# Kernel optimization log

Hardware: AMD Instinct MI355X
Metric: run time of the kernel (lower is better)

Reference implementation:

```python
import jax, jax.numpy as jnp
import numpy as np

B, N, C = 16, 256, 2048
CLASSES = (16, 5, 5)
H = len(CLASSES)
EPS = 1e-5


def setup_inputs() -> dict:
    key = jax.random.key(0)
    ks = iter(jax.random.split(key, 32))
    d = {}
    d["features"] = jax.random.normal(next(ks), (B, N, C), dtype=jnp.float32)
    # 3 hidden conv layers per head; 3x3 conv on 1x1 spatial == linear with center tap.
    # Stack the H heads' weights: [H, C_out, C_in].
    std = 1.0 / np.sqrt(C)
    for i in (1, 2, 3):
        d[f"W{i}"] = jax.random.normal(next(ks), (H, C, C), dtype=jnp.float32) * std
        d[f"g{i}"] = 1.0 + 0.1 * jax.random.normal(next(ks), (H, C), dtype=jnp.float32)
        d[f"b{i}"] = 0.1 * jax.random.normal(next(ks), (H, C), dtype=jnp.float32)
        d[f"m{i}"] = 0.1 * jax.random.normal(next(ks), (H, C), dtype=jnp.float32)
        d[f"v{i}"] = jax.random.uniform(next(ks), (H, C), dtype=jnp.float32, minval=0.5, maxval=1.5)
    # Final 1x1 conv per head: [c_i, C] weight + [c_i] bias (output dims differ per head).
    for h, c in enumerate(CLASSES):
        d[f"Wf{h}"] = jax.random.normal(next(ks), (c, C), dtype=jnp.float32) * std
        d[f"bf{h}"] = 0.1 * jax.random.normal(next(ks), (c,), dtype=jnp.float32)
    return d


def _bn_relu(y, g, b, m, v):
    # y: [H, M, C]; per-head inference-mode BN folded to scale/shift, then ReLU.
    scale = g / jnp.sqrt(v + EPS)          # [H, C]
    shift = b - m * scale                  # [H, C]
    return jax.nn.relu(y * scale[:, None, :] + shift[:, None, :])


def reference(features, W1, g1, b1, m1, v1, W2, g2, b2, m2, v2, W3, g3, b3, m3, v3,
              Wf0, bf0, Wf1, bf1, Wf2, bf2):
    Bs, Ns, Cs = features.shape
    x = features.reshape(Bs * Ns, Cs)                       # [M, C]
    y = jnp.einsum("mc,hdc->hmd", x, W1)                    # [H, M, C]
    y = _bn_relu(y, g1, b1, m1, v1)
    y = jnp.einsum("hmc,hdc->hmd", y, W2)
    y = _bn_relu(y, g2, b2, m2, v2)
    y = jnp.einsum("hmc,hdc->hmd", y, W3)
    y = _bn_relu(y, g3, b3, m3, v3)
    outs = [y[h] @ Wf.T + bf for h, (Wf, bf) in enumerate([(Wf0, bf0), (Wf1, bf1), (Wf2, bf2)])]
    cl = jnp.concatenate(outs, axis=-1)                     # [M, sum(classes)]
    return cl.reshape(Bs, Ns, cl.shape[-1])
```

## Files before the change

### kernel.cpp

```cpp
#include <hip/hip_runtime.h>
#include <hip/hip_bf16.h>

typedef __attribute__((ext_vector_type(8))) short short8;
typedef __attribute__((ext_vector_type(4))) float f32x4;

#define BN_EPS 1e-5f
#define MROWS 4096
#define CDIM 2048
#define NKT 32

#define SB() __builtin_amdgcn_sched_barrier(0)

__device__ __forceinline__ void gload_lds16(const void* g, void* l) {
  __builtin_amdgcn_global_load_lds(
      (const __attribute__((address_space(1))) void*)g,
      (__attribute__((address_space(3))) void*)l, 16, 0, 0);
}

__global__ __launch_bounds__(256) void cvt_f32_bf16(const float* __restrict__ in,
                                                    unsigned short* __restrict__ out,
                                                    int n4) {
  int idx = blockIdx.x * blockDim.x + threadIdx.x;
  int stride = gridDim.x * blockDim.x;
  for (int i = idx; i < n4; i += stride) {
    float4 vv = ((const float4*)in)[i];
    __hip_bfloat16 h0 = __float2bfloat16(vv.x);
    __hip_bfloat16 h1 = __float2bfloat16(vv.y);
    __hip_bfloat16 h2 = __float2bfloat16(vv.z);
    __hip_bfloat16 h3 = __float2bfloat16(vv.w);
    ushort4 o;
    o.x = *(unsigned short*)&h0;
    o.y = *(unsigned short*)&h1;
    o.z = *(unsigned short*)&h2;
    o.w = *(unsigned short*)&h3;
    ((ushort4*)out)[i] = o;
  }
}

__global__ __launch_bounds__(512, 2) void gemm256_bn_relu(
    const __hip_bfloat16* __restrict__ A, long long a_hstride,
    const __hip_bfloat16* __restrict__ W,
    const float* __restrict__ gp, const float* __restrict__ bp,
    const float* __restrict__ mp, const float* __restrict__ vp,
    __hip_bfloat16* __restrict__ out)
{
  __shared__ __hip_bfloat16 sm[65536];

  const int tid  = threadIdx.x;
  const int w    = tid >> 6;
  const int lane = tid & 63;

  const int bid = blockIdx.x;
  const int swz = (bid & 7) * 48 + (bid >> 3);
  const int h   = swz >> 7;
  const int mt  = (swz & 127) >> 3;
  const int nt  = swz & 7;

  const __hip_bfloat16* Abase = A + (size_t)h * (size_t)a_hstride + (size_t)(mt * 256) * CDIM;
  const __hip_bfloat16* Bbase = W + ((size_t)h * CDIM + (size_t)(nt * 256)) * CDIM;

  const int slot0 = w * 128 + lane;
  const int srow  = slot0 >> 3;
  const int gcol  = ((slot0 & 7) ^ (srow & 7)) << 3;

  const int wm = w >> 2;
  const int wn = w & 3;
  const int fr = lane & 15;
  const int fg = lane >> 4;
  const int offs0 = fr * 64 + ((fg ^ (fr & 7)) << 3);
  const int offs1 = fr * 64 + (((fg + 4) ^ (fr & 7)) << 3);
  const int aOff = wm * 8192;
  const int bOff = 16384 + (wn >> 1) * 8192 + (wn & 1) * 4096;

  auto STAGE = [&](int dbuf, int mat, int ih, int t) {
    const __hip_bfloat16* sp = (mat ? Bbase : Abase)
        + (size_t)(ih * 128 + srow) * CDIM + t * 64 + gcol;
    __hip_bfloat16* dp = &sm[dbuf * 32768 + mat * 16384 + ih * 8192 + w * 1024];
    gload_lds16(sp, dp);
    gload_lds16(sp + 8 * CDIM, dp + 512);
  };

  f32x4 acc[8][4] = {};
  short8 A0[4], A1[4], B0[2], B1[2];

  const __hip_bfloat16* aB[2] = { &sm[aOff], &sm[32768 + aOff] };
  const __hip_bfloat16* bB[2] = { &sm[bOff], &sm[32768 + bOff] };

#define LDA(dst, base, i0, offs)                                        \
  _Pragma("unroll") for (int i_ = 0; i_ < 4; ++i_)                      \
    dst[i_] = *(const short8*)((base) + ((i0) + i_) * 1024 + (offs));
#define LDB(dst, base, j0, offs)                                        \
  _Pragma("unroll") for (int j_ = 0; j_ < 2; ++j_)                      \
    dst[j_] = *(const short8*)((base) + ((j0) + j_) * 1024 + (offs));

#define MFMA_Q(ioff, joff, Aset, Bset)                                  \
  __builtin_amdgcn_s_setprio(1);                                        \
  _Pragma("unroll") for (int i_ = 0; i_ < 4; ++i_)                      \
  _Pragma("unroll") for (int j_ = 0; j_ < 2; ++j_)                      \
    acc[i_ + ioff][j_ + joff] = __builtin_amdgcn_mfma_f32_16x16x32_bf16( \
        Aset[i_], Bset[j_], acc[i_ + ioff][j_ + joff], 0, 0, 0);        \
  __builtin_amdgcn_s_setprio(0);

  STAGE(0, 0, 0, 0); STAGE(0, 0, 1, 0); STAGE(0, 1, 0, 0); STAGE(0, 1, 1, 0);
  STAGE(1, 0, 0, 1);
  asm volatile("s_waitcnt vmcnt(2)" ::: "memory");
  SB();
  __builtin_amdgcn_s_barrier();
  SB();
  LDA(A0, aB[0], 0, offs0);
  LDA(A1, aB[0], 4, offs0);
  LDB(B0, bB[0], 0, offs0);
  LDB(B1, bB[0], 2, offs0);
  SB();

#pragma unroll 2
  for (int t = 0; t < NKT - 1; ++t) {
    const int d = t & 1, dn = d ^ 1;
    const __hip_bfloat16* aHd = aB[d];
    const __hip_bfloat16* bHd = bB[d];
    const __hip_bfloat16* aHn = aB[dn];
    const __hip_bfloat16* bHn = bB[dn];

    MFMA_Q(0, 0, A0, B0); SB();
    STAGE(dn, 0, 1, t + 1); SB();
    MFMA_Q(0, 2, A0, B1); SB();
    LDA(A0, aHd, 0, offs1); SB();
    MFMA_Q(4, 0, A1, B0); SB();
    STAGE(dn, 1, 0, t + 1);
    LDB(B0, bHd, 0, offs1); SB();
    MFMA_Q(4, 2, A1, B1); SB();
    STAGE(dn, 1, 1, t + 1);
    LDB(B1, bHd, 2, offs1);
    LDA(A1, aHd, 4, offs1); SB();
    MFMA_Q(0, 0, A0, B0); SB();
    if (t + 2 < NKT) { STAGE(d, 0, 0, t + 2); }
    SB();
    MFMA_Q(0, 2, A0, B1); SB();
    if (t + 2 < NKT) { asm volatile("s_waitcnt vmcnt(6)" ::: "memory"); }
    else             { asm volatile("s_waitcnt vmcnt(4)" ::: "memory"); }
    SB();
    __builtin_amdgcn_s_barrier();
    SB();
    LDA(A0, aHn, 0, offs0); SB();
    MFMA_Q(4, 0, A1, B0); SB();
    if (t + 2 < NKT) { asm volatile("s_waitcnt vmcnt(2)" ::: "memory"); }
    else             { asm volatile("s_waitcnt vmcnt(0)" ::: "memory"); }
    SB();
    __builtin_amdgcn_s_barrier();
    SB();
    LDB(B0, bHn, 0, offs0); SB();
    MFMA_Q(4, 2, A1, B1); SB();
    LDB(B1, bHn, 2, offs0);
    LDA(A1, aHn, 4, offs0); SB();
  }

  {
    const int d = (NKT - 1) & 1;
    const __hip_bfloat16* aHd = aB[d];
    const __hip_bfloat16* bHd = bB[d];
    MFMA_Q(0, 0, A0, B0); SB();
    MFMA_Q(0, 2, A0, B1); SB();
    LDA(A0, aHd, 0, offs1); SB();
    MFMA_Q(4, 0, A1, B0); SB();
    LDB(B0, bHd, 0, offs1); SB();
    MFMA_Q(4, 2, A1, B1); SB();
    LDB(B1, bHd, 2, offs1);
    LDA(A1, aHd, 4, offs1); SB();
    MFMA_Q(0, 0, A0, B0); SB();
    MFMA_Q(0, 2, A0, B1); SB();
    MFMA_Q(4, 0, A1, B0); SB();
    MFMA_Q(4, 2, A1, B1); SB();
  }

  const float* gh = gp + h * CDIM;
  const float* bh = bp + h * CDIM;
  const float* mh = mp + h * CDIM;
  const float* vh = vp + h * CDIM;
  const int colBase = nt * 256 + wn * 64 + fr;
  const int rowBase = mt * 256 + wm * 128 + fg * 4;
#pragma unroll
  for (int j = 0; j < 4; ++j) {
    const int col = colBase + j * 16;
    const float sc = gh[col] / sqrtf(vh[col] + BN_EPS);
    const float sh = bh[col] - mh[col] * sc;
#pragma unroll
    for (int i = 0; i < 8; ++i) {
      const int row = rowBase + i * 16;
#pragma unroll
      for (int rr = 0; rr < 4; ++rr) {
        float val = acc[i][j][rr] * sc + sh;
        val = val > 0.f ? val : 0.f;
        out[((size_t)h * MROWS + row + rr) * CDIM + col] = __float2bfloat16(val);
      }
    }
  }
}

__global__ __launch_bounds__(256) void pack_wf(
    const float* __restrict__ Wf0, const float* __restrict__ Wf1,
    const float* __restrict__ Wf2, __hip_bfloat16* __restrict__ Wfb) {
  int idx = blockIdx.x * 256 + threadIdx.x;
  if (idx >= 3 * 16 * CDIM) return;
  int h = idx / (16 * CDIM);
  int rem = idx - h * 16 * CDIM;
  int j = rem / CDIM;
  int k = rem - j * CDIM;
  float v = 0.f;
  if (h == 0)            v = Wf0[j * CDIM + k];
  else if (h == 1)       { if (j < 5) v = Wf1[j * CDIM + k]; }
  else                   { if (j < 5) v = Wf2[j * CDIM + k]; }
  Wfb[idx] = __float2bfloat16(v);
}

__global__ __launch_bounds__(512) void final_mfma(
    const __hip_bfloat16* __restrict__ act,
    const __hip_bfloat16* __restrict__ Wfb,
    const float* __restrict__ bf0, const float* __restrict__ bf1,
    const float* __restrict__ bf2, float* __restrict__ out)
{
  __shared__ float red[8][3][256];
  const int tid  = threadIdx.x;
  const int w    = tid >> 6;
  const int lane = tid & 63;
  const int r0   = blockIdx.x * 16;
  const int fr   = lane & 15;
  const int fk   = (lane >> 4) * 8;
  const int kbase = w * 256 + fk;

  f32x4 acc[3] = {};
  const __hip_bfloat16* aRow = act + (size_t)(r0 + fr) * CDIM + kbase;
  const __hip_bfloat16* bRow = Wfb + (size_t)fr * CDIM + kbase;
#pragma unroll
  for (int ks = 0; ks < 8; ++ks) {
    const int k = ks * 32;
#pragma unroll
    for (int h = 0; h < 3; ++h) {
      short8 a = *(const short8*)(aRow + (size_t)h * MROWS * CDIM + k);
      short8 b = *(const short8*)(bRow + h * 16 * CDIM + k);
      acc[h] = __builtin_amdgcn_mfma_f32_16x16x32_bf16(a, b, acc[h], 0, 0, 0);
    }
  }

  const int rb = (lane >> 4) * 4;
#pragma unroll
  for (int h = 0; h < 3; ++h)
#pragma unroll
    for (int r = 0; r < 4; ++r)
      red[w][h][(rb + r) * 16 + fr] = acc[h][r];
  __syncthreads();

  for (int e = tid; e < 768; e += 512) {
    const int h = e >> 8, idx = e & 255;
    const int row = idx >> 4, col = idx & 15;
    float s = 0.f;
#pragma unroll
    for (int w2 = 0; w2 < 8; ++w2) s += red[w2][h][idx];
    float* orow = out + (size_t)(r0 + row) * 26;
    if (h == 0)                 orow[col]      = s + bf0[col];
    else if (h == 1) { if (col < 5) orow[16 + col] = s + bf1[col]; }
    else             { if (col < 5) orow[21 + col] = s + bf2[col]; }
  }
}

extern "C" void kernel_launch(void* const* d_in, const int* in_sizes, int n_in,
                              void* d_out, int out_size, void* d_ws, size_t ws_size,
                              hipStream_t stream) {
  const float* feat = (const float*)d_in[0];
  const float* W1 = (const float*)d_in[1];
  const float* g1 = (const float*)d_in[2];
  const float* b1 = (const float*)d_in[3];
  const float* m1 = (const float*)d_in[4];
  const float* v1 = (const float*)d_in[5];
  const float* W2 = (const float*)d_in[6];
  const float* g2 = (const float*)d_in[7];
  const float* b2 = (const float*)d_in[8];
  const float* m2 = (const float*)d_in[9];
  const float* v2 = (const float*)d_in[10];
  const float* W3 = (const float*)d_in[11];
  const float* g3 = (const float*)d_in[12];
  const float* b3 = (const float*)d_in[13];
  const float* m3 = (const float*)d_in[14];
  const float* v3 = (const float*)d_in[15];
  const float* Wf0 = (const float*)d_in[16];
  const float* bf0 = (const float*)d_in[17];
  const float* Wf1 = (const float*)d_in[18];
  const float* bf1 = (const float*)d_in[19];
  const float* Wf2 = (const float*)d_in[20];
  const float* bf2 = (const float*)d_in[21];
  float* out = (float*)d_out;

  char* ws = (char*)d_ws;
  __hip_bfloat16* wbuf = (__hip_bfloat16*)ws;
  __hip_bfloat16* actA = (__hip_bfloat16*)(ws + 25165824);
  __hip_bfloat16* actB = (__hip_bfloat16*)(ws + 25165824 + 50331648);
  __hip_bfloat16* xb   = actB;
  __hip_bfloat16* Wfb  = wbuf;

  const int nW4 = (3 * CDIM * CDIM) / 4;
  const int nX4 = (MROWS * CDIM) / 4;
  const long long hstride = (long long)MROWS * CDIM;

  cvt_f32_bf16<<<2048, 256, 0, stream>>>(feat, (unsigned short*)xb, nX4);

  cvt_f32_bf16<<<2048, 256, 0, stream>>>(W1, (unsigned short*)wbuf, nW4);
  gemm256_bn_relu<<<384, 512, 0, stream>>>(xb, 0LL, wbuf, g1, b1, m1, v1, actA);

  cvt_f32_bf16<<<2048, 256, 0, stream>>>(W2, (unsigned short*)wbuf, nW4);
  gemm256_bn_relu<<<384, 512, 0, stream>>>(actA, hstride, wbuf, g2, b2, m2, v2, actB);

  cvt_f32_bf16<<<2048, 256, 0, stream>>>(W3, (unsigned short*)wbuf, nW4);
  gemm256_bn_relu<<<384, 512, 0, stream>>>(actB, hstride, wbuf, g3, b3, m3, v3, actA);

  pack_wf<<<384, 256, 0, stream>>>(Wf0, Wf1, Wf2, Wfb);
  final_mfma<<<256, 512, 0, stream>>>(actA, Wfb, bf0, bf1, bf2, out);
}
```

Before: 361.1 us.

## Replace 256x256 GEMM tile with 128x256 tile and triple-buffered K=32 pipeline

Rewrites the three hidden-layer GEMM kernels to use 128x256 output tiles with a K-step of 32, a triple-buffered LDS ring, and a simpler schedule of one barrier per step. This doubles the grid to 768 blocks and targets higher occupancy (launch bounds 4), with the aim of filling the 256 CUs better than 384 large tiles do. In exchange, per-block data reuse is lower (A is reread more often), there are twice as many K iterations with more barriers, and the hand-tuned interleaving of MFMA and LDS loads is lost.

```diff
diff --git a/kernel.cpp b/kernel.cpp
--- a/kernel.cpp
+++ b/kernel.cpp
@@ -7,7 +7,6 @@
 #define BN_EPS 1e-5f
 #define MROWS 4096
 #define CDIM 2048
-#define NKT 32
 
 #define SB() __builtin_amdgcn_sched_barrier(0)
 
@@ -37,139 +36,82 @@
   }
 }
 
-__global__ __launch_bounds__(512, 2) void gemm256_bn_relu(
+__global__ __launch_bounds__(512, 4) void gemm128_bn_relu(
     const __hip_bfloat16* __restrict__ A, long long a_hstride,
     const __hip_bfloat16* __restrict__ W,
     const float* __restrict__ gp, const float* __restrict__ bp,
     const float* __restrict__ mp, const float* __restrict__ vp,
     __hip_bfloat16* __restrict__ out)
 {
-  __shared__ __hip_bfloat16 sm[65536];
+  __shared__ __hip_bfloat16 sm[36864];
 
   const int tid  = threadIdx.x;
   const int w    = tid >> 6;
   const int lane = tid & 63;
 
   const int bid = blockIdx.x;
-  const int swz = (bid & 7) * 48 + (bid >> 3);
-  const int h   = swz >> 7;
-  const int mt  = (swz & 127) >> 3;
-  const int nt  = swz & 7;
-
-  const __hip_bfloat16* Abase = A + (size_t)h * (size_t)a_hstride + (size_t)(mt * 256) * CDIM;
+  const int swz = (bid & 7) * 96 + (bid >> 3);
+  const int h   = swz >> 8;
+  const int rem = swz & 255;
+  const int mt  = rem >> 3;
+  const int nt  = rem & 7;
+
+  const __hip_bfloat16* Abase = A + (size_t)h * (size_t)a_hstride + (size_t)(mt * 128) * CDIM;
   const __hip_bfloat16* Bbase = W + ((size_t)h * CDIM + (size_t)(nt * 256)) * CDIM;
 
-  const int slot0 = w * 128 + lane;
-  const int srow  = slot0 >> 3;
-  const int gcol  = ((slot0 & 7) ^ (srow & 7)) << 3;
-
-  const int wm = w >> 2;
-  const int wn = w & 3;
-  const int fr = lane & 15;
-  const int fg = lane >> 4;
-  const int offs0 = fr * 64 + ((fg ^ (fr & 7)) << 3);
-  const int offs1 = fr * 64 + (((fg + 4) ^ (fr & 7)) << 3);
-  const int aOff = wm * 8192;
-  const int bOff = 16384 + (wn >> 1) * 8192 + (wn & 1) * 4096;
-
-  auto STAGE = [&](int dbuf, int mat, int ih, int t) {
-    const __hip_bfloat16* sp = (mat ? Bbase : Abase)
-        + (size_t)(ih * 128 + srow) * CDIM + t * 64 + gcol;
-    __hip_bfloat16* dp = &sm[dbuf * 32768 + mat * 16384 + ih * 8192 + w * 1024];
-    gload_lds16(sp, dp);
-    gload_lds16(sp + 8 * CDIM, dp + 512);
+  const int rowA = tid >> 2;
+  const int chA  = (tid & 3) ^ ((rowA >> 1) & 3);
+  const __hip_bfloat16* aSrc  = Abase + (size_t)rowA * CDIM + chA * 8;
+  const __hip_bfloat16* bSrc0 = Bbase + (size_t)rowA * CDIM + chA * 8;
+  const __hip_bfloat16* bSrc1 = bSrc0 + (size_t)128 * CDIM;
+
+  const int wm = w >> 2, wn = w & 3;
+  const int fr = lane & 15, fg = lane >> 4;
+  const int cadj  = (fg ^ ((fr >> 1) & 3)) * 8;
+  const int abase = (wm * 64 + fr) * 32 + cadj;
+  const int bbase = 4096 + (wn * 64 + fr) * 32 + cadj;
+
+  auto STAGE = [&](int off, int t) {
+    __hip_bfloat16* dp = &sm[off + tid * 8];
+    gload_lds16(aSrc  + t * 32, dp);
+    gload_lds16(bSrc0 + t * 32, dp + 4096);
+    gload_lds16(bSrc1 + t * 32, dp + 8192);
   };
 
-  f32x4 acc[8][4] = {};
-  short8 A0[4], A1[4], B0[2], B1[2];
-
-  const __hip_bfloat16* aB[2] = { &sm[aOff], &sm[32768 + aOff] };
-  const __hip_bfloat16* bB[2] = { &sm[bOff], &sm[32768 + bOff] };
-
-#define LDA(dst, base, i0, offs)                                        \
-  _Pragma("unroll") for (int i_ = 0; i_ < 4; ++i_)                      \
-    dst[i_] = *(const short8*)((base) + ((i0) + i_) * 1024 + (offs));
-#define LDB(dst, base, j0, offs)                                        \
-  _Pragma("unroll") for (int j_ = 0; j_ < 2; ++j_)                      \
-    dst[j_] = *(const short8*)((base) + ((j0) + j_) * 1024 + (offs));
-
-#define MFMA_Q(ioff, joff, Aset, Bset)                                  \
-  __builtin_amdgcn_s_setprio(1);                                        \
-  _Pragma("unroll") for (int i_ = 0; i_ < 4; ++i_)                      \
-  _Pragma("unroll") for (int j_ = 0; j_ < 2; ++j_)                      \
-    acc[i_ + ioff][j_ + joff] = __builtin_amdgcn_mfma_f32_16x16x32_bf16( \
-        Aset[i_], Bset[j_], acc[i_ + ioff][j_ + joff], 0, 0, 0);        \
-  __builtin_amdgcn_s_setprio(0);
-
-  STAGE(0, 0, 0, 0); STAGE(0, 0, 1, 0); STAGE(0, 1, 0, 0); STAGE(0, 1, 1, 0);
-  STAGE(1, 0, 0, 1);
-  asm volatile("s_waitcnt vmcnt(2)" ::: "memory");
+  f32x4 acc[4][4] = {};
+
+  STAGE(0, 0);
+  STAGE(12288, 1);
+  asm volatile("s_waitcnt vmcnt(3)" ::: "memory");
   SB();
   __builtin_amdgcn_s_barrier();
   SB();
-  LDA(A0, aB[0], 0, offs0);
-  LDA(A1, aB[0], 4, offs0);
-  LDB(B0, bB[0], 0, offs0);
-  LDB(B1, bB[0], 2, offs0);
-  SB();
-
-#pragma unroll 2
-  for (int t = 0; t < NKT - 1; ++t) {
-    const int d = t & 1, dn = d ^ 1;
-    const __hip_bfloat16* aHd = aB[d];
-    const __hip_bfloat16* bHd = bB[d];
-    const __hip_bfloat16* aHn = aB[dn];
-    const __hip_bfloat16* bHn = bB[dn];
-
-    MFMA_Q(0, 0, A0, B0); SB();
-    STAGE(dn, 0, 1, t + 1); SB();
-    MFMA_Q(0, 2, A0, B1); SB();
-    LDA(A0, aHd, 0, offs1); SB();
-    MFMA_Q(4, 0, A1, B0); SB();
-    STAGE(dn, 1, 0, t + 1);
-    LDB(B0, bHd, 0, offs1); SB();
-    MFMA_Q(4, 2, A1, B1); SB();
-    STAGE(dn, 1, 1, t + 1);
-    LDB(B1, bHd, 2, offs1);
-    LDA(A1, aHd, 4, offs1); SB();
-    MFMA_Q(0, 0, A0, B0); SB();
-    if (t + 2 < NKT) { STAGE(d, 0, 0, t + 2); }
+
+  int oc = 0, on = 12288, os = 24576;
+  for (int t = 0; t < 64; ++t) {
+    if (t + 2 < 64) STAGE(os, t + 2);
     SB();
-    MFMA_Q(0, 2, A0, B1); SB();
-    if (t + 2 < NKT) { asm volatile("s_waitcnt vmcnt(6)" ::: "memory"); }
-    else             { asm volatile("s_waitcnt vmcnt(4)" ::: "memory"); }
+    short8 af[4], bf_[4];
+#pragma unroll
+    for (int i = 0; i < 4; ++i) af[i]  = *(const short8*)&sm[oc + abase + i * 512];
+#pragma unroll
+    for (int j = 0; j < 4; ++j) bf_[j] = *(const short8*)&sm[oc + bbase + j * 512];
+    __builtin_amdgcn_s_setprio(1);
+#pragma unroll
+    for (int i = 0; i < 4; ++i)
+#pragma unroll
+      for (int j = 0; j < 4; ++j)
+        acc[i][j] = __builtin_amdgcn_mfma_f32_16x16x32_bf16(af[i], bf_[j], acc[i][j], 0, 0, 0);
+    __builtin_amdgcn_s_setprio(0);
     SB();
-    __builtin_amdgcn_s_barrier();
-    SB();
-    LDA(A0, aHn, 0, offs0); SB();
-    MFMA_Q(4, 0, A1, B0); SB();
-    if (t + 2 < NKT) { asm volatile("s_waitcnt vmcnt(2)" ::: "memory"); }
-    else             { asm volatile("s_waitcnt vmcnt(0)" ::: "memory"); }
-    SB();
-    __builtin_amdgcn_s_barrier();
-    SB();
-    LDB(B0, bHn, 0, offs0); SB();
-    MFMA_Q(4, 2, A1, B1); SB();
-    LDB(B1, bHn, 2, offs0);
-    LDA(A1, aHn, 4, offs0); SB();
-  }
-
-  {
-    const int d = (NKT - 1) & 1;
-    const __hip_bfloat16* aHd = aB[d];
-    const __hip_bfloat16* bHd = bB[d];
-    MFMA_Q(0, 0, A0, B0); SB();
-    MFMA_Q(0, 2, A0, B1); SB();
-    LDA(A0, aHd, 0, offs1); SB();
-    MFMA_Q(4, 0, A1, B0); SB();
-    LDB(B0, bHd, 0, offs1); SB();
-    MFMA_Q(4, 2, A1, B1); SB();
-    LDB(B1, bHd, 2, offs1);
-    LDA(A1, aHd, 4, offs1); SB();
-    MFMA_Q(0, 0, A0, B0); SB();
-    MFMA_Q(0, 2, A0, B1); SB();
-    MFMA_Q(4, 0, A1, B0); SB();
-    MFMA_Q(4, 2, A1, B1); SB();
+    if (t < 63) {
+      if (t + 2 < 64) { asm volatile("s_waitcnt vmcnt(3)" ::: "memory"); }
+      else            { asm volatile("s_waitcnt vmcnt(0)" ::: "memory"); }
+      SB();
+      __builtin_amdgcn_s_barrier();
+      SB();
+    }
+    const int tmp = oc; oc = on; on = os; os = tmp;
   }
 
   const float* gh = gp + h * CDIM;
@@ -177,14 +119,14 @@
   const float* mh = mp + h * CDIM;
   const float* vh = vp + h * CDIM;
   const int colBase = nt * 256 + wn * 64 + fr;
-  const int rowBase = mt * 256 + wm * 128 + fg * 4;
+  const int rowBase = mt * 128 + wm * 64 + fg * 4;
 #pragma unroll
   for (int j = 0; j < 4; ++j) {
     const int col = colBase + j * 16;
     const float sc = gh[col] / sqrtf(vh[col] + BN_EPS);
     const float sh = bh[col] - mh[col] * sc;
 #pragma unroll
-    for (int i = 0; i < 8; ++i) {
+    for (int i = 0; i < 4; ++i) {
       const int row = rowBase + i * 16;
 #pragma unroll
       for (int rr = 0; rr < 4; ++rr) {
@@ -303,13 +245,13 @@
   cvt_f32_bf16<<<2048, 256, 0, stream>>>(feat, (unsigned short*)xb, nX4);
 
   cvt_f32_bf16<<<2048, 256, 0, stream>>>(W1, (unsigned short*)wbuf, nW4);
-  gemm256_bn_relu<<<384, 512, 0, stream>>>(xb, 0LL, wbuf, g1, b1, m1, v1, actA);
+  gemm128_bn_relu<<<768, 512, 0, stream>>>(xb, 0LL, wbuf, g1, b1, m1, v1, actA);
 
   cvt_f32_bf16<<<2048, 256, 0, stream>>>(W2, (unsigned short*)wbuf, nW4);
-  gemm256_bn_relu<<<384, 512, 0, stream>>>(actA, hstride, wbuf, g2, b2, m2, v2, actB);
+  gemm128_bn_relu<<<768, 512, 0, stream>>>(actA, hstride, wbuf, g2, b2, m2, v2, actB);
 
   cvt_f32_bf16<<<2048, 256, 0, stream>>>(W3, (unsigned short*)wbuf, nW4);
-  gemm256_bn_relu<<<384, 512, 0, stream>>>(actB, hstride, wbuf, g3, b3, m3, v3, actA);
+  gemm128_bn_relu<<<768, 512, 0, stream>>>(actB, hstride, wbuf, g3, b3, m3, v3, actA);
 
   pack_wf<<<384, 256, 0, stream>>>(Wf0, Wf1, Wf2, Wfb);
   final_mfma<<<256, 512, 0, stream>>>(actA, Wfb, bf0, bf1, bf2, out);
```

Measured after the change: 389.8 us. +7.9%, slower.
